# Optimization experiments

Hardware: AMD Instinct MI355X
Metric: run time of the kernel (lower is better)

## Reference

```python
import jax, jax.numpy as jnp
import numpy as np

B, S, D = 4, 2048, 4096
E, R, OUT = 4, 64, 4096
NUM_MOD, NUM_REG, HID = 4, 3, 128
ALPHA = 128.0
SCALING = ALPHA / R  # alpha / rank = 2.0
BALANCE_COEFF = 0.01


def setup_inputs() -> dict:
    key = jax.random.key(0)
    ks = jax.random.split(key, 8)
    return {
        "x": jax.random.normal(ks[0], (B, S, D), jnp.float32),
        "reliability_vec": jax.random.uniform(ks[1], (B, NUM_MOD), jnp.float32),
        "regime_vec": jax.random.uniform(ks[2], (B, NUM_REG), jnp.float32),
        # LoRA experts stacked: A ~ N(0, 1/rank), B random (torch inits B=0; randomized here for a non-trivial baseline)
        "lora_A": jax.random.normal(ks[3], (E, R, D), jnp.float32) / np.sqrt(R).astype(np.float32),
        "lora_B": jax.random.normal(ks[4], (E, OUT, R), jnp.float32) * 0.02,
        # router: Linear(4103->128) -> GELU -> Linear(128->4)
        "w1": jax.random.normal(ks[5], (D + NUM_MOD + NUM_REG, HID), jnp.float32) * 0.02,
        "b1": jnp.zeros((HID,), jnp.float32),
        "w2": jax.random.normal(ks[6], (HID, E), jnp.float32) * 0.02,
        "b2": jnp.zeros((E,), jnp.float32),
    }


def reference(x, reliability_vec, regime_vec, lora_A, lora_B, w1, b1, w2, b2):
    # Router on pooled features + degradation context
    x_pooled = x.mean(axis=1)                                   # [B, D]
    router_in = jnp.concatenate([x_pooled, reliability_vec, regime_vec], axis=-1)
    h = jax.nn.gelu(router_in @ w1 + b1)                        # [B, HID]
    gate_logits = h @ w2 + b2                                   # [B, E]
    gate_probs = jax.nn.softmax(gate_logits, axis=-1)
    top_expert = jnp.argmax(gate_probs, axis=-1)                # [B] int

    # Sparse top-1 dispatch (eval path): gather each sample's expert weights
    A_sel = lora_A[top_expert]                                  # [B, R, D]
    B_sel = lora_B[top_expert]                                  # [B, OUT, R]
    xr = jnp.einsum('bsd,brd->bsr', x, A_sel)                   # [B, S, R]
    out = jnp.einsum('bsr,bor->bso', xr, B_sel) * SCALING       # [B, S, OUT]

    avg_gate = gate_probs.mean(axis=0)
    balance_loss = BALANCE_COEFF * (E * jnp.sum(avg_gate ** 2))
    return out, balance_loss
```

## Files before the change

### kernel.cpp

```cpp
#include <hip/hip_runtime.h>

constexpr int B_ = 4, S_ = 2048, D_ = 4096, E_ = 4, R_ = 64, OUT_ = 4096;
constexpr int NMOD = 4, NREG = 3, HID_ = 128;
constexpr int RIN_ = D_ + NMOD + NREG;
constexpr float SCALING_ = 2.0f;
constexpr int SB_  = 64;
constexpr int NSB_ = S_ / SB_;
constexpr int KQ_  = 4;
constexpr int KCH_ = D_ / KQ_;
constexpr int KC_  = 33;
constexpr size_t XRN_ = (size_t)E_ * B_ * S_ * R_;

constexpr size_t WS_PP    = 0;
constexpr size_t WS_HACC2 = WS_PP + (size_t)NSB_ * B_ * D_;
constexpr size_t WS_TOP   = WS_HACC2 + B_ * KC_ * HID_;
constexpr size_t WS_ABF   = WS_TOP + 16;
constexpr size_t WS_BBF   = WS_ABF + (size_t)E_ * R_ * D_ / 2;
constexpr size_t WS_XRP   = WS_BBF + (size_t)E_ * OUT_ * R_ / 2;
constexpr size_t WS_XRB   = WS_XRP + KQ_ * XRN_;

using short8 = __attribute__((ext_vector_type(8))) short;
using f32x4  = __attribute__((ext_vector_type(4))) float;

__device__ inline unsigned short f2bf(float f) {
    unsigned u = __float_as_uint(f);
    unsigned r = u + 0x7FFFu + ((u >> 16) & 1u);
    return (unsigned short)(r >> 16);
}

__global__ void cvt_w_kernel(const float* __restrict__ A, const float* __restrict__ Bw,
                             ushort* __restrict__ Abf, ushort* __restrict__ Bbf) {
    int i = blockIdx.x * blockDim.x + threadIdx.x;
    constexpr int N4 = E_ * R_ * D_ / 4;
    if (i < N4) {
        float4 v = ((const float4*)A)[i];
        ((ushort4*)Abf)[i] = make_ushort4(f2bf(v.x), f2bf(v.y), f2bf(v.z), f2bf(v.w));
    } else {
        int j = i - N4;
        float4 v = ((const float4*)Bw)[j];
        ((ushort4*)Bbf)[j] = make_ushort4(f2bf(v.x), f2bf(v.y), f2bf(v.z), f2bf(v.w));
    }
}

__global__ __launch_bounds__(256, 3) void xpool_kernel(const float* __restrict__ x,
                                                       const ushort* __restrict__ Abf,
                                                       float* __restrict__ pool_part,
                                                       float* __restrict__ xr_part) {
    __shared__ ushort xs[SB_][72];
    __shared__ ushort as[E_][64][72];
    __shared__ float4 red2[4][16];
    int b = blockIdx.y, sb = blockIdx.x, kq = blockIdx.z;
    int s0 = sb * SB_;
    int t = threadIdx.x, lane = t & 63, w = t >> 6;
    const float* xb = x + ((size_t)b * S_ + s0) * D_;
    int xrow = t >> 4, xfq = t & 15;
    f32x4 acc[E_][4] = {};
    for (int kc = 0; kc < KCH_ / 64; ++kc) {
        int k0 = kq * KCH_ + kc * 64;
        float4 v0 = *(const float4*)(xb + (size_t)xrow * D_ + k0 + xfq * 4);
        float4 v1 = *(const float4*)(xb + (size_t)(xrow + 16) * D_ + k0 + xfq * 4);
        float4 v2 = *(const float4*)(xb + (size_t)(xrow + 32) * D_ + k0 + xfq * 4);
        float4 v3 = *(const float4*)(xb + (size_t)(xrow + 48) * D_ + k0 + xfq * 4);
        *(ushort4*)&xs[xrow][xfq * 4]      = make_ushort4(f2bf(v0.x), f2bf(v0.y), f2bf(v0.z), f2bf(v0.w));
        *(ushort4*)&xs[xrow + 16][xfq * 4] = make_ushort4(f2bf(v1.x), f2bf(v1.y), f2bf(v1.z), f2bf(v1.w));
        *(ushort4*)&xs[xrow + 32][xfq * 4] = make_ushort4(f2bf(v2.x), f2bf(v2.y), f2bf(v2.z), f2bf(v2.w));
        *(ushort4*)&xs[xrow + 48][xfq * 4] = make_ushort4(f2bf(v3.x), f2bf(v3.y), f2bf(v3.z), f2bf(v3.w));
        float4 v = make_float4(v0.x + v1.x + v2.x + v3.x, v0.y + v1.y + v2.y + v3.y,
                               v0.z + v1.z + v2.z + v3.z, v0.w + v1.w + v2.w + v3.w);
#pragma unroll
        for (int j = 0; j < 8; ++j) {
            int lin = t + 256 * j;
            int e = lin >> 9, rr = (lin >> 3) & 63, cq = lin & 7;
            int4 av = *(const int4*)(Abf + ((size_t)e * R_ + rr) * D_ + k0 + cq * 8);
            *(int4*)&as[e][rr][cq * 8] = av;
        }
        v.x += __shfl_xor(v.x, 16); v.y += __shfl_xor(v.y, 16);
        v.z += __shfl_xor(v.z, 16); v.w += __shfl_xor(v.w, 16);
        v.x += __shfl_xor(v.x, 32); v.y += __shfl_xor(v.y, 32);
        v.z += __shfl_xor(v.z, 32); v.w += __shfl_xor(v.w, 32);
        if (lane < 16) red2[w][lane] = v;
        __syncthreads();
        if (t < 16) {
            float4 s = red2[0][t], r1 = red2[1][t], r2 = red2[2][t], r3 = red2[3][t];
            s.x += r1.x + r2.x + r3.x; s.y += r1.y + r2.y + r3.y;
            s.z += r1.z + r2.z + r3.z; s.w += r1.w + r2.w + r3.w;
            *(float4*)&pool_part[(size_t)sb * (B_ * D_) + b * D_ + k0 + t * 4] = s;
        }
        int mrow = w * 16 + (lane & 15);
        int koff = (lane >> 4) * 8;
#pragma unroll
        for (int kk = 0; kk < 2; ++kk) {
            short8 af = *(const short8*)&xs[mrow][kk * 32 + koff];
#pragma unroll
            for (int e = 0; e < E_; ++e)
#pragma unroll
                for (int n = 0; n < 4; ++n) {
                    short8 bf = *(const short8*)&as[e][n * 16 + (lane & 15)][kk * 32 + koff];
                    acc[e][n] = __builtin_amdgcn_mfma_f32_16x16x32_bf16(af, bf, acc[e][n], 0, 0, 0);
                }
        }
        __syncthreads();
    }
    int col0 = lane & 15;
    int rb   = w * 16 + ((lane >> 4) << 2);
#pragma unroll
    for (int e = 0; e < E_; ++e) {
        float* xo = xr_part + (size_t)kq * (E_ * B_ * S_ * R_) +
                    (((size_t)e * B_ + b) * S_ + s0) * R_;
#pragma unroll
        for (int n = 0; n < 4; ++n)
#pragma unroll
            for (int i = 0; i < 4; ++i)
                xo[(size_t)(rb + i) * R_ + n * 16 + col0] = acc[e][n][i];
    }
}

__global__ __launch_bounds__(256) void xr_red_kernel(const float* __restrict__ xr_part,
                                                     ushort* __restrict__ xr_bf) {
    size_t i = (size_t)blockIdx.x * 256 + threadIdx.x;
    constexpr size_t STR = XRN_ / 4;
    float4 s = ((const float4*)xr_part)[i];
    float4 a = ((const float4*)xr_part)[i + STR];
    float4 c = ((const float4*)xr_part)[i + 2 * STR];
    float4 d = ((const float4*)xr_part)[i + 3 * STR];
    s.x += a.x + c.x + d.x; s.y += a.y + c.y + d.y;
    s.z += a.z + c.z + d.z; s.w += a.w + c.w + d.w;
    ((ushort4*)xr_bf)[i] = make_ushort4(f2bf(s.x), f2bf(s.y), f2bf(s.z), f2bf(s.w));
}

__global__ __launch_bounds__(256) void router_h_kernel(const float* __restrict__ pool_part,
                                                       const float* __restrict__ rel,
                                                       const float* __restrict__ reg,
                                                       const float* __restrict__ w1,
                                                       float* __restrict__ hacc2) {
    __shared__ float rin[128];
    __shared__ float red[256];
    int b = blockIdx.x, kc = blockIdx.y;
    int t = threadIdx.x;
    int k0 = kc * 128;
    if (t < 128) {
        int k = k0 + t;
        float v = 0.f;
        if (k < D_) {
            float s = 0.f;
            for (int p = 0; p < NSB_; ++p) s += pool_part[(size_t)p * (B_ * D_) + b * D_ + k];
            v = s * (1.0f / S_);
        } else if (k < D_ + NMOD) v = rel[b * NMOD + (k - D_)];
        else if (k < RIN_)        v = reg[b * NREG + (k - D_ - NMOD)];
        rin[t] = v;
    }
    __syncthreads();
    int h = t & 127, half = t >> 7;
    float acc = 0.f;
#pragma unroll 8
    for (int i = 0; i < 64; ++i) {
        int kk = 2 * i + half;
        int k = k0 + kk;
        if (k < RIN_) acc += rin[kk] * w1[(size_t)k * HID_ + h];
    }
    red[t] = acc;
    __syncthreads();
    if (t < 128)
        hacc2[((size_t)b * KC_ + kc) * HID_ + t] = red[t] + red[t + 128];
}

__global__ void router_finish_kernel(const float* __restrict__ hacc2, const float* __restrict__ b1,
                                     const float* __restrict__ w2, const float* __restrict__ b2,
                                     int* __restrict__ top, float* __restrict__ bal_out) {
    __shared__ float h_lds[B_][HID_];
    __shared__ float logit[B_][E_];
    __shared__ float probs[B_][E_];
    int t = threadIdx.x;
    for (int b = 0; b < B_; ++b) {
        float v = b1[t];
        for (int j = 0; j < KC_; ++j) v += hacc2[((size_t)b * KC_ + j) * HID_ + t];
        float u = 0.7978845608028654f * (v + 0.044715f * v * v * v);
        h_lds[b][t] = 0.5f * v * (1.0f + tanhf(u));
    }
    __syncthreads();
    if (t < B_ * E_) {
        int b = t >> 2, e = t & 3;
        float acc = b2[e];
        for (int j = 0; j < HID_; ++j) acc += h_lds[b][j] * w2[j * E_ + e];
        logit[b][e] = acc;
    }
    __syncthreads();
    if (t < B_) {
        int b = t;
        float m = logit[b][0]; int arg = 0;
        for (int e = 1; e < E_; ++e) if (logit[b][e] > m) { m = logit[b][e]; arg = e; }
        float s = 0.f, p[E_];
        for (int e = 0; e < E_; ++e) { p[e] = expf(logit[b][e] - m); s += p[e]; }
        for (int e = 0; e < E_; ++e) probs[b][e] = p[e] / s;
        top[b] = arg;
    }
    __syncthreads();
    if (t == 0) {
        float bal = 0.f;
        for (int e = 0; e < E_; ++e) {
            float avg = 0.25f * (probs[0][e] + probs[1][e] + probs[2][e] + probs[3][e]);
            bal += avg * avg;
        }
        *bal_out = 0.01f * E_ * bal;
    }
}

__global__ __launch_bounds__(256) void out_kernel(const ushort* __restrict__ xr_bf,
                                                  const ushort* __restrict__ Bbf,
                                                  const int* __restrict__ top,
                                                  float* __restrict__ out) {
    __shared__ ushort xrs[64][72];
    __shared__ ushort bs[128][72];
    int b  = blockIdx.z;
    int e  = top[b];
    int s0 = blockIdx.x * 64, o0 = blockIdx.y * 128;
    int t = threadIdx.x, lane = t & 63, w = t >> 6;
    const ushort* xrb = xr_bf + (((size_t)e * B_ + b) * S_ + s0) * R_;
#pragma unroll
    for (int i = 0; i < 2; ++i) {
        int lin = t + 256 * i; int row = lin >> 3, cq = lin & 7;
        int4 v = *(const int4*)(xrb + (size_t)row * R_ + cq * 8);
        *(int4*)&xrs[row][cq * 8] = v;
    }
    const ushort* Bb = Bbf + (size_t)e * OUT_ * R_ + (size_t)o0 * R_;
#pragma unroll
    for (int i = 0; i < 4; ++i) {
        int lin = t + 256 * i; int row = lin >> 3, cq = lin & 7;
        int4 v = *(const int4*)(Bb + (size_t)row * R_ + cq * 8);
        *(int4*)&bs[row][cq * 8] = v;
    }
    __syncthreads();
    int mrow = w * 16 + (lane & 15);
    int koff = (lane >> 4) * 8;
    f32x4 acc[8] = {};
#pragma unroll
    for (int kk = 0; kk < 2; ++kk) {
        short8 af = *(const short8*)&xrs[mrow][kk * 32 + koff];
#pragma unroll
        for (int n = 0; n < 8; ++n) {
            short8 bf = *(const short8*)&bs[n * 16 + (lane & 15)][kk * 32 + koff];
            acc[n] = __builtin_amdgcn_mfma_f32_16x16x32_bf16(af, bf, acc[n], 0, 0, 0);
        }
    }
    int col0  = lane & 15;
    int rbase = (lane >> 4) << 2;
    float* ob = out + ((size_t)b * S_ + s0 + w * 16) * OUT_ + o0;
#pragma unroll
    for (int n = 0; n < 8; ++n)
#pragma unroll
        for (int i = 0; i < 4; ++i)
            ob[(size_t)(rbase + i) * OUT_ + n * 16 + col0] = acc[n][i] * SCALING_;
}

extern "C" void kernel_launch(void* const* d_in, const int* in_sizes, int n_in,
                              void* d_out, int out_size, void* d_ws, size_t ws_size,
                              hipStream_t stream) {
    const float* x   = (const float*)d_in[0];
    const float* rel = (const float*)d_in[1];
    const float* reg = (const float*)d_in[2];
    const float* lA  = (const float*)d_in[3];
    const float* lB  = (const float*)d_in[4];
    const float* w1  = (const float*)d_in[5];
    const float* b1  = (const float*)d_in[6];
    const float* w2  = (const float*)d_in[7];
    const float* b2  = (const float*)d_in[8];
    float* out = (float*)d_out;
    float* ws  = (float*)d_ws;

    float*  pp    = ws + WS_PP;
    float*  hacc2 = ws + WS_HACC2;
    int*    top   = (int*)(ws + WS_TOP);
    ushort* Abf   = (ushort*)(ws + WS_ABF);
    ushort* Bbf   = (ushort*)(ws + WS_BBF);
    float*  xrp   = ws + WS_XRP;
    ushort* xrb   = (ushort*)(ws + WS_XRB);

    cvt_w_kernel<<<2 * (E_ * R_ * D_ / 4) / 256, 256, 0, stream>>>(lA, lB, Abf, Bbf);
    xpool_kernel<<<dim3(NSB_, B_, KQ_), 256, 0, stream>>>(x, Abf, pp, xrp);
    xr_red_kernel<<<(int)(XRN_ / 4 / 256), 256, 0, stream>>>(xrp, xrb);
    router_h_kernel<<<dim3(B_, KC_), 256, 0, stream>>>(pp, rel, reg, w1, hacc2);
    router_finish_kernel<<<1, 128, 0, stream>>>(hacc2, b1, w2, b2, top,
                                                out + (size_t)out_size - 1);
    out_kernel<<<dim3(S_ / 64, OUT_ / 128, B_), 256, 0, stream>>>(xrb, Bbf, top, out);
}
```

Before: 135.5 us.

## Split xr projection by expert instead of K, drop split-K reduction kernel

Restructures the x·A projection so each block covers one expert over the full D range instead of all four experts over a quarter of D. This removes the fp32 split-K partial buffer and the separate reduction kernel, and bf16 xr is written directly. It also uses 512-thread blocks with register prefetch of the next K chunk. The cost is that x is now read (and converted to bf16) once per expert, four times in total, instead of once per K-quarter.

```diff
diff --git a/kernel.cpp b/kernel.cpp
--- a/kernel.cpp
+++ b/kernel.cpp
@@ -6,18 +6,14 @@
 constexpr float SCALING_ = 2.0f;
 constexpr int SB_  = 64;
 constexpr int NSB_ = S_ / SB_;
-constexpr int KQ_  = 4;
-constexpr int KCH_ = D_ / KQ_;
 constexpr int KC_  = 33;
-constexpr size_t XRN_ = (size_t)E_ * B_ * S_ * R_;
 
 constexpr size_t WS_PP    = 0;
 constexpr size_t WS_HACC2 = WS_PP + (size_t)NSB_ * B_ * D_;
 constexpr size_t WS_TOP   = WS_HACC2 + B_ * KC_ * HID_;
 constexpr size_t WS_ABF   = WS_TOP + 16;
 constexpr size_t WS_BBF   = WS_ABF + (size_t)E_ * R_ * D_ / 2;
-constexpr size_t WS_XRP   = WS_BBF + (size_t)E_ * OUT_ * R_ / 2;
-constexpr size_t WS_XRB   = WS_XRP + KQ_ * XRN_;
+constexpr size_t WS_XRB   = WS_BBF + (size_t)E_ * OUT_ * R_ / 2;
 
 using short8 = __attribute__((ext_vector_type(8))) short;
 using f32x4  = __attribute__((ext_vector_type(4))) float;
@@ -42,90 +38,74 @@
     }
 }
 
-__global__ __launch_bounds__(256, 3) void xpool_kernel(const float* __restrict__ x,
-                                                       const ushort* __restrict__ Abf,
-                                                       float* __restrict__ pool_part,
-                                                       float* __restrict__ xr_part) {
+__global__ __launch_bounds__(512, 4) void xe_kernel(const float* __restrict__ x,
+                                                    const ushort* __restrict__ Abf,
+                                                    float* __restrict__ pool_part,
+                                                    ushort* __restrict__ xr_bf) {
     __shared__ ushort xs[SB_][72];
-    __shared__ ushort as[E_][64][72];
-    __shared__ float4 red2[4][16];
-    int b = blockIdx.y, sb = blockIdx.x, kq = blockIdx.z;
+    __shared__ ushort as[R_][72];
+    __shared__ float4 red2[8][16];
+    int sb = blockIdx.x, b = blockIdx.y, e = blockIdx.z;
     int s0 = sb * SB_;
     int t = threadIdx.x, lane = t & 63, w = t >> 6;
-    const float* xb = x + ((size_t)b * S_ + s0) * D_;
+    int m = w & 3, p = w >> 2;
+    const float*  xb = x   + ((size_t)b * S_ + s0) * D_;
+    const ushort* Ab = Abf + (size_t)e * R_ * D_;
     int xrow = t >> 4, xfq = t & 15;
-    f32x4 acc[E_][4] = {};
-    for (int kc = 0; kc < KCH_ / 64; ++kc) {
-        int k0 = kq * KCH_ + kc * 64;
-        float4 v0 = *(const float4*)(xb + (size_t)xrow * D_ + k0 + xfq * 4);
-        float4 v1 = *(const float4*)(xb + (size_t)(xrow + 16) * D_ + k0 + xfq * 4);
-        float4 v2 = *(const float4*)(xb + (size_t)(xrow + 32) * D_ + k0 + xfq * 4);
-        float4 v3 = *(const float4*)(xb + (size_t)(xrow + 48) * D_ + k0 + xfq * 4);
+    int arow = t >> 3, acq = t & 7;
+    float4 v0 = *(const float4*)(xb + (size_t)xrow * D_ + xfq * 4);
+    float4 v1 = *(const float4*)(xb + (size_t)(xrow + 32) * D_ + xfq * 4);
+    int4  av  = *(const int4*)(Ab + (size_t)arow * D_ + acq * 8);
+    f32x4 acc[2] = {};
+    int mrow = m * 16 + (lane & 15);
+    int koff = (lane >> 4) * 8;
+    for (int kc = 0; kc < D_ / 64; ++kc) {
+        __syncthreads();
         *(ushort4*)&xs[xrow][xfq * 4]      = make_ushort4(f2bf(v0.x), f2bf(v0.y), f2bf(v0.z), f2bf(v0.w));
-        *(ushort4*)&xs[xrow + 16][xfq * 4] = make_ushort4(f2bf(v1.x), f2bf(v1.y), f2bf(v1.z), f2bf(v1.w));
-        *(ushort4*)&xs[xrow + 32][xfq * 4] = make_ushort4(f2bf(v2.x), f2bf(v2.y), f2bf(v2.z), f2bf(v2.w));
-        *(ushort4*)&xs[xrow + 48][xfq * 4] = make_ushort4(f2bf(v3.x), f2bf(v3.y), f2bf(v3.z), f2bf(v3.w));
-        float4 v = make_float4(v0.x + v1.x + v2.x + v3.x, v0.y + v1.y + v2.y + v3.y,
-                               v0.z + v1.z + v2.z + v3.z, v0.w + v1.w + v2.w + v3.w);
-#pragma unroll
-        for (int j = 0; j < 8; ++j) {
-            int lin = t + 256 * j;
-            int e = lin >> 9, rr = (lin >> 3) & 63, cq = lin & 7;
-            int4 av = *(const int4*)(Abf + ((size_t)e * R_ + rr) * D_ + k0 + cq * 8);
-            *(int4*)&as[e][rr][cq * 8] = av;
-        }
-        v.x += __shfl_xor(v.x, 16); v.y += __shfl_xor(v.y, 16);
-        v.z += __shfl_xor(v.z, 16); v.w += __shfl_xor(v.w, 16);
-        v.x += __shfl_xor(v.x, 32); v.y += __shfl_xor(v.y, 32);
-        v.z += __shfl_xor(v.z, 32); v.w += __shfl_xor(v.w, 32);
-        if (lane < 16) red2[w][lane] = v;
+        *(ushort4*)&xs[xrow + 32][xfq * 4] = make_ushort4(f2bf(v1.x), f2bf(v1.y), f2bf(v1.z), f2bf(v1.w));
+        *(int4*)&as[arow][acq * 8] = av;
+        if (e == 0) {
+            float4 v = make_float4(v0.x + v1.x, v0.y + v1.y, v0.z + v1.z, v0.w + v1.w);
+            v.x += __shfl_xor(v.x, 16); v.y += __shfl_xor(v.y, 16);
+            v.z += __shfl_xor(v.z, 16); v.w += __shfl_xor(v.w, 16);
+            v.x += __shfl_xor(v.x, 32); v.y += __shfl_xor(v.y, 32);
+            v.z += __shfl_xor(v.z, 32); v.w += __shfl_xor(v.w, 32);
+            if (lane < 16) red2[w][lane] = v;
+        }
         __syncthreads();
-        if (t < 16) {
-            float4 s = red2[0][t], r1 = red2[1][t], r2 = red2[2][t], r3 = red2[3][t];
-            s.x += r1.x + r2.x + r3.x; s.y += r1.y + r2.y + r3.y;
-            s.z += r1.z + r2.z + r3.z; s.w += r1.w + r2.w + r3.w;
-            *(float4*)&pool_part[(size_t)sb * (B_ * D_) + b * D_ + k0 + t * 4] = s;
-        }
-        int mrow = w * 16 + (lane & 15);
-        int koff = (lane >> 4) * 8;
+        if (e == 0 && t < 16) {
+            float4 s = red2[0][t];
+#pragma unroll
+            for (int j = 1; j < 8; ++j) {
+                float4 r = red2[j][t];
+                s.x += r.x; s.y += r.y; s.z += r.z; s.w += r.w;
+            }
+            *(float4*)&pool_part[(size_t)sb * (B_ * D_) + b * D_ + kc * 64 + t * 4] = s;
+        }
+        if (kc < D_ / 64 - 1) {
+            int k0n = (kc + 1) * 64;
+            v0 = *(const float4*)(xb + (size_t)xrow * D_ + k0n + xfq * 4);
+            v1 = *(const float4*)(xb + (size_t)(xrow + 32) * D_ + k0n + xfq * 4);
+            av = *(const int4*)(Ab + (size_t)arow * D_ + k0n + acq * 8);
+        }
 #pragma unroll
         for (int kk = 0; kk < 2; ++kk) {
             short8 af = *(const short8*)&xs[mrow][kk * 32 + koff];
 #pragma unroll
-            for (int e = 0; e < E_; ++e)
-#pragma unroll
-                for (int n = 0; n < 4; ++n) {
-                    short8 bf = *(const short8*)&as[e][n * 16 + (lane & 15)][kk * 32 + koff];
-                    acc[e][n] = __builtin_amdgcn_mfma_f32_16x16x32_bf16(af, bf, acc[e][n], 0, 0, 0);
-                }
-        }
-        __syncthreads();
+            for (int n = 0; n < 2; ++n) {
+                short8 bf = *(const short8*)&as[(p * 2 + n) * 16 + (lane & 15)][kk * 32 + koff];
+                acc[n] = __builtin_amdgcn_mfma_f32_16x16x32_bf16(af, bf, acc[n], 0, 0, 0);
+            }
+        }
     }
     int col0 = lane & 15;
-    int rb   = w * 16 + ((lane >> 4) << 2);
-#pragma unroll
-    for (int e = 0; e < E_; ++e) {
-        float* xo = xr_part + (size_t)kq * (E_ * B_ * S_ * R_) +
-                    (((size_t)e * B_ + b) * S_ + s0) * R_;
-#pragma unroll
-        for (int n = 0; n < 4; ++n)
-#pragma unroll
-            for (int i = 0; i < 4; ++i)
-                xo[(size_t)(rb + i) * R_ + n * 16 + col0] = acc[e][n][i];
-    }
-}
-
-__global__ __launch_bounds__(256) void xr_red_kernel(const float* __restrict__ xr_part,
-                                                     ushort* __restrict__ xr_bf) {
-    size_t i = (size_t)blockIdx.x * 256 + threadIdx.x;
-    constexpr size_t STR = XRN_ / 4;
-    float4 s = ((const float4*)xr_part)[i];
-    float4 a = ((const float4*)xr_part)[i + STR];
-    float4 c = ((const float4*)xr_part)[i + 2 * STR];
-    float4 d = ((const float4*)xr_part)[i + 3 * STR];
-    s.x += a.x + c.x + d.x; s.y += a.y + c.y + d.y;
-    s.z += a.z + c.z + d.z; s.w += a.w + c.w + d.w;
-    ((ushort4*)xr_bf)[i] = make_ushort4(f2bf(s.x), f2bf(s.y), f2bf(s.z), f2bf(s.w));
+    int rb   = m * 16 + ((lane >> 4) << 2);
+    ushort* xo = xr_bf + (((size_t)e * B_ + b) * S_ + s0) * R_;
+#pragma unroll
+    for (int n = 0; n < 2; ++n)
+#pragma unroll
+        for (int i = 0; i < 4; ++i)
+            xo[(size_t)(rb + i) * R_ + (p * 2 + n) * 16 + col0] = f2bf(acc[n][i]);
 }
 
 __global__ __launch_bounds__(256) void router_h_kernel(const float* __restrict__ pool_part,
@@ -272,12 +252,10 @@
     int*    top   = (int*)(ws + WS_TOP);
     ushort* Abf   = (ushort*)(ws + WS_ABF);
     ushort* Bbf   = (ushort*)(ws + WS_BBF);
-    float*  xrp   = ws + WS_XRP;
     ushort* xrb   = (ushort*)(ws + WS_XRB);
 
     cvt_w_kernel<<<2 * (E_ * R_ * D_ / 4) / 256, 256, 0, stream>>>(lA, lB, Abf, Bbf);
-    xpool_kernel<<<dim3(NSB_, B_, KQ_), 256, 0, stream>>>(x, Abf, pp, xrp);
-    xr_red_kernel<<<(int)(XRN_ / 4 / 256), 256, 0, stream>>>(xrp, xrb);
+    xe_kernel<<<dim3(NSB_, B_, E_), 512, 0, stream>>>(x, Abf, pp, xrb);
     router_h_kernel<<<dim3(B_, KC_), 256, 0, stream>>>(pp, rel, reg, w1, hacc2);
     router_finish_kernel<<<1, 128, 0, stream>>>(hacc2, b1, w2, b2, top,
                                                 out + (size_t)out_size - 1);
```

Measured after the change: 133.3 us. Within noise of the previous version (-1.6%).
